# Kernel optimization log

Hardware: AMD Instinct MI355X
Metric: run time of the kernel (lower is better)

## Reference

```python
import jax, jax.numpy as jnp
import numpy as np

N_USER, N_ITEM, N_KNOW, HIDDEN, BATCH = 200000, 20000, 128, 256, 16384
N_EDGES = 2 * N_KNOW - 3  # chain edges (k-1,k) k=1..K-1 then skip edges (k-2,k) k=2..K-1


def setup_inputs() -> dict:
    key = jax.random.key(0)
    ks = jax.random.split(key, 12)
    return {
        'user_ids': jax.random.randint(ks[0], (BATCH,), 0, N_USER),
        'item_ids': jax.random.randint(ks[1], (BATCH,), 0, N_ITEM),
        'item_know': (jax.random.uniform(ks[2], (BATCH, N_KNOW)) < 0.5).astype(jnp.float32),
        'priori': jax.random.normal(ks[3], (N_USER, N_KNOW), jnp.float32),
        'condi_p': jax.random.normal(ks[4], (N_USER, N_EDGES), jnp.float32),
        'condi_n': jax.random.normal(ks[5], (N_USER, N_EDGES), jnp.float32),
        'item_diff_w': jax.random.normal(ks[6], (N_ITEM, N_KNOW), jnp.float32),
        'item_disc_w': jax.random.normal(ks[7], (N_ITEM, 1), jnp.float32),
        'Wu': jax.random.normal(ks[8], (HIDDEN, N_KNOW), jnp.float32) * 0.05,
        'bu': jax.random.normal(ks[9], (HIDDEN,), jnp.float32) * 0.05,
        'Wi': jax.random.normal(ks[10], (HIDDEN, N_KNOW), jnp.float32) * 0.05,
        'bi': jax.random.normal(ks[11], (HIDDEN,), jnp.float32) * 0.05,
    }


def _posterior(bp, bcp, bcn):
    # bp: [B,K] sigmoid(priori rows); bcp/bcn: [B,E] sigmoid(condi rows).
    # Topological DAG propagation. For node k the torch code sums over all
    # 2^len_p predecessor bitmasks of prod_j(mask_j*margin_p_j + (1-mask_j)*margin_n_j),
    # which factorizes exactly to prod_j(margin_p_j + margin_n_j) (same math).
    K = bp.shape[1]
    p0 = bp[:, 0]                               # node 0: no predecessors
    p1 = bcp[:, 0] * p0 + bcn[:, 0] * (1.0 - p0)  # node 1: pred {0}, exponent 1/1
    # nodes k>=2 have sorted preds {k-2, k-1}; edge (k-1,k) -> col k-1, edge (k-2,k) -> col (K-1)+(k-2)
    cp_b, cn_b = bcp[:, 1:K - 1].T, bcn[:, 1:K - 1].T      # (k-1,k) edges, [K-2,B]
    cp_a, cn_a = bcp[:, K - 1:].T, bcn[:, K - 1:].T        # (k-2,k) edges, [K-2,B]

    def step(carry, x):
        p_km2, p_km1 = carry
        cpa, cna, cpb, cnb = x
        # pow(condi, 1/len_p) with len_p=2 -> sqrt
        ta = jnp.sqrt(cpa) * p_km2 + jnp.sqrt(cna) * (1.0 - p_km2)
        tb = jnp.sqrt(cpb) * p_km1 + jnp.sqrt(cnb) * (1.0 - p_km1)
        pk = ta * tb
        return (p_km1, pk), pk

    _, rest = jax.lax.scan(step, (p0, p1), (cp_a, cn_a, cp_b, cn_b))  # rest: [K-2,B]
    return jnp.concatenate([p0[:, None], p1[:, None], rest.T], axis=1)  # [B,K]


def reference(user_ids, item_ids, item_know, priori, condi_p, condi_n,
              item_diff_w, item_disc_w, Wu, bu, Wi, bi):
    bp = jax.nn.sigmoid(priori[user_ids])      # [B,K]
    bcp = jax.nn.sigmoid(condi_p[user_ids])    # [B,E]
    bcn = jax.nn.sigmoid(condi_n[user_ids])
    mastery = _posterior(bp, bcp, bcn)         # [B,K]
    idiff = jax.nn.sigmoid(item_diff_w[item_ids])  # [B,K]
    idisc = jax.nn.sigmoid(item_disc_w[item_ids])  # [B,1]
    user_factor = jnp.tanh((mastery * item_know) @ Wu.T + bu)      # [B,H]
    item_factor = jax.nn.sigmoid((idiff * item_know) @ Wi.T + bi)  # [B,H]
    # mirt2pl: 1/(1+exp(-sum(u*i) + offset)) == sigmoid(sum - offset)
    logits = jnp.sum(user_factor * item_factor, axis=1, keepdims=True) - idisc
    return jax.nn.sigmoid(logits)  # [B,1]
```

## Files before the change

### kernel.cpp

```cpp
#include <hip/hip_runtime.h>

#define BATCH   16384
#define NKNOW   128
#define NEDGE   253
#define RPB     16

typedef __attribute__((ext_vector_type(8))) short  s16x8;
typedef __attribute__((ext_vector_type(4))) float  f32x4;
typedef __attribute__((ext_vector_type(4))) int    i32x4;

typedef unsigned short u16;
typedef unsigned int   u32;
typedef unsigned long long u64;

__device__ __forceinline__ float sigm(float x) { return 1.0f / (1.0f + __expf(-x)); }

__device__ __forceinline__ u16 f2bf_rn(float x) {
    u32 u = __float_as_uint(x);
    u += 0x7FFFu + ((u >> 16) & 1u);
    return (u16)(u >> 16);
}
__device__ __forceinline__ float bf2f(u16 h) { return __uint_as_float(((u32)h) << 16); }

__global__ __launch_bounds__(256, 4) void prep2(
    const int*   __restrict__ user_ids,
    const int*   __restrict__ item_ids,
    const float* __restrict__ item_know,
    const float* __restrict__ priori,
    const float* __restrict__ condi_p,
    const float* __restrict__ condi_n,
    const float* __restrict__ item_diff_w,
    const float* __restrict__ Wu,
    const float* __restrict__ Wi,
    u16*         __restrict__ wsp,
    u32*         __restrict__ mhi32,
    u32*         __restrict__ mlo32,
    u16*         __restrict__ dhi,
    u16*         __restrict__ dlo)
{
    __shared__ float4 sP[16][127];
    __shared__ uint4  sMask[16];

    const int tid = threadIdx.x;
    const int wid = tid >> 6, j = tid & 63;
    const int r0  = blockIdx.x * 16;

    #pragma unroll 2
    for (int q = 0; q < 4; ++q) {
        const int r = wid * 4 + q, row = r0 + r;
        const int uid = user_ids[row], iid = item_ids[row];
        const float* cp = condi_p + (size_t)uid * NEDGE;
        const float* cn = condi_n + (size_t)uid * NEDGE;
        const float* kw = item_know   + (size_t)row * NKNOW;
        const float* dw = item_diff_w + (size_t)iid * NKNOW;

        float a0p = cp[127 + j], a0n = cn[127 + j], b0p = cp[1 + j], b0n = cn[1 + j];
        float a1p = 0.f, a1n = 0.f, b1p = 0.f, b1n = 0.f;
        if (j < 62) { a1p = cp[191 + j]; a1n = cn[191 + j]; b1p = cp[65 + j]; b1n = cn[65 + j]; }
        float k0 = kw[j], k1 = kw[64 + j];
        float d0 = dw[j], d1 = dw[64 + j];

        float4 sA;
        sA.x = sqrtf(sigm(a0p)); sA.y = sqrtf(sigm(a0n));
        sA.z = sqrtf(sigm(b0p)); sA.w = sqrtf(sigm(b0n));
        sP[r][1 + j] = sA;
        if (j < 62) {
            float4 sB;
            sB.x = sqrtf(sigm(a1p)); sB.y = sqrtf(sigm(a1n));
            sB.z = sqrtf(sigm(b1p)); sB.w = sqrtf(sigm(b1n));
            sP[r][65 + j] = sB;
        }

        float dv0 = sigm(d0) * k0, dv1 = sigm(d1) * k1;
        u16 h0 = f2bf_rn(dv0), h1 = f2bf_rn(dv1);
        dhi[(size_t)row * NKNOW + j]      = h0;
        dhi[(size_t)row * NKNOW + 64 + j] = h1;
        dlo[(size_t)row * NKNOW + j]      = f2bf_rn(dv0 - bf2f(h0));
        dlo[(size_t)row * NKNOW + 64 + j] = f2bf_rn(dv1 - bf2f(h1));

        u64 m0 = __ballot(k0 > 0.5f);
        u64 m1 = __ballot(k1 > 0.5f);
        if (j == 0) {
            float4 hd;
            hd.x = sigm(cp[0]); hd.y = sigm(cn[0]);
            hd.z = sigm(priori[(size_t)uid * NKNOW]); hd.w = 0.f;
            sP[r][0] = hd;
            uint4 mm; mm.x = (u32)m0; mm.y = (u32)(m0 >> 32);
            mm.z = (u32)m1; mm.w = (u32)(m1 >> 32);
            sMask[r] = mm;
        }
    }

    if (blockIdx.x < 256) {
        int i = blockIdx.x * 256 + tid;
        bool isU = i < 32768;
        int  jj  = isU ? i : i - 32768;
        float w  = isU ? Wu[jj] : Wi[jj];
        u16 h = f2bf_rn(w);
        u16 l = f2bf_rn(w - bf2f(h));
        int base = isU ? 0 : 65536;
        wsp[base + jj]         = h;
        wsp[base + 32768 + jj] = l;
    }
    __syncthreads();

    if (tid < 16) {
        const int r = tid, row = r0 + r;
        uint4 mm = sMask[r];
        const u64 b0 = (u64)mm.x | ((u64)mm.y << 32);
        const u64 b1 = (u64)mm.z | ((u64)mm.w << 32);
        u32* mh = mhi32 + (size_t)row * 64;
        u32* ml = mlo32 + (size_t)row * 64;

        float4 h = sP[r][0];
        float p0 = h.z;
        float p1 = fmaf(p0, h.x - h.y, h.y);
        {
            float v0 = (b0 & 1ull) ? p0 : 0.f;
            float v1 = (b0 & 2ull) ? p1 : 0.f;
            u16 q0 = f2bf_rn(v0), q1 = f2bf_rn(v1);
            mh[0] = (u32)q0 | ((u32)q1 << 16);
            ml[0] = (u32)f2bf_rn(v0 - bf2f(q0)) | ((u32)f2bf_rn(v1 - bf2f(q1)) << 16);
        }

        float pm2 = p0, pm1 = p1, pendm = 0.f;
        float4 A[7], Bv[7];

#define LOADB(buf, bi_)                                               \
    _Pragma("unroll")                                                 \
    for (int t = 0; t < 7; ++t) buf[t] = sP[r][1 + 7 * (bi_) + t];

#define STEPS(buf, bi_)                                               \
    _Pragma("unroll")                                                 \
    for (int t = 0; t < 7; ++t) {                                     \
        const int k = 2 + 7 * (bi_) + t;                              \
        float4 s = buf[t];                                            \
        float ta = fmaf(pm2, s.x - s.y, s.y);                         \
        float tb = fmaf(pm1, s.z - s.w, s.w);                         \
        float pk = ta * tb;                                           \
        bool bit = (k < 64) ? ((b0 >> k) & 1ull) : ((b1 >> (k - 64)) & 1ull); \
        float pkm = bit ? pk : 0.f;                                   \
        if (k & 1) {                                                  \
            u16 q0 = f2bf_rn(pendm), q1 = f2bf_rn(pkm);               \
            mh[k >> 1] = (u32)q0 | ((u32)q1 << 16);                   \
            ml[k >> 1] = (u32)f2bf_rn(pendm - bf2f(q0)) |             \
                         ((u32)f2bf_rn(pkm - bf2f(q1)) << 16);        \
        } else pendm = pkm;                                           \
        pm2 = pm1; pm1 = pk;                                          \
    }
        LOADB(A, 0);
        LOADB(Bv, 1);  STEPS(A, 0);
        LOADB(A, 2);   STEPS(Bv, 1);
        LOADB(Bv, 3);  STEPS(A, 2);
        LOADB(A, 4);   STEPS(Bv, 3);
        LOADB(Bv, 5);  STEPS(A, 4);
        LOADB(A, 6);   STEPS(Bv, 5);
        LOADB(Bv, 7);  STEPS(A, 6);
        LOADB(A, 8);   STEPS(Bv, 7);
        LOADB(Bv, 9);  STEPS(A, 8);
        LOADB(A, 10);  STEPS(Bv, 9);
        LOADB(Bv, 11); STEPS(A, 10);
        LOADB(A, 12);  STEPS(Bv, 11);
        LOADB(Bv, 13); STEPS(A, 12);
        LOADB(A, 14);  STEPS(Bv, 13);
        LOADB(Bv, 15); STEPS(A, 14);
        LOADB(A, 16);  STEPS(Bv, 15);
        LOADB(Bv, 17); STEPS(A, 16);
        STEPS(Bv, 17);
#undef LOADB
#undef STEPS
    }
}

__global__ __launch_bounds__(256, 2) void gemm_ncd(
    const int*   __restrict__ item_ids,
    const float* __restrict__ item_disc_w,
    const float* __restrict__ bu,
    const float* __restrict__ bi,
    const u16*   __restrict__ wsp,
    const u32*   __restrict__ mhi32,
    const u32*   __restrict__ mlo32,
    const u32*   __restrict__ dhi32,
    const u32*   __restrict__ dlo32,
    float*       __restrict__ out)
{
    __shared__ float sRed[4][32];

    const int tid  = threadIdx.x;
    const int lane = tid & 63;
    const int wid  = tid >> 6;
    const int l15  = lane & 15, lq = lane >> 4;
    const int r0   = blockIdx.x * 32;

    const u16* WuH = wsp;
    const u16* WuL = wsp + 32768;
    const u16* WiH = wsp + 65536;
    const u16* WiL = wsp + 98304;

    float rowsum[2][4] = {{0.f,0.f,0.f,0.f},{0.f,0.f,0.f,0.f}};

    #pragma unroll 1
    for (int t = 0; t < 4; ++t) {
        const int hcol = wid * 64 + t * 16 + l15;
        s16x8 uh[4], ul[4], ih[4], il[4];
        #pragma unroll
        for (int kc = 0; kc < 4; ++kc) {
            const int ke = kc * 32 + lq * 8;
            uh[kc] = *(const s16x8*)(WuH + hcol * NKNOW + ke);
            ul[kc] = *(const s16x8*)(WuL + hcol * NKNOW + ke);
            ih[kc] = *(const s16x8*)(WiH + hcol * NKNOW + ke);
            il[kc] = *(const s16x8*)(WiL + hcol * NKNOW + ke);
        }
        const float bub = bu[hcol], bib = bi[hcol];

        #pragma unroll
        for (int rg = 0; rg < 2; ++rg) {
            const int row = r0 + rg * 16 + l15;
            f32x4 accU = {0.f, 0.f, 0.f, 0.f};
            f32x4 accV = {0.f, 0.f, 0.f, 0.f};
            #pragma unroll
            for (int kc = 0; kc < 4; ++kc) {
                const int aoff = row * 64 + kc * 16 + lq * 4;
                s16x8 mh = *(const s16x8*)(mhi32 + aoff);
                s16x8 mlv = *(const s16x8*)(mlo32 + aoff);
                s16x8 dh = *(const s16x8*)(dhi32 + aoff);
                s16x8 dl = *(const s16x8*)(dlo32 + aoff);
                accU = __builtin_amdgcn_mfma_f32_16x16x32_bf16(mh, uh[kc], accU, 0, 0, 0);
                accU = __builtin_amdgcn_mfma_f32_16x16x32_bf16(mh, ul[kc], accU, 0, 0, 0);
                accU = __builtin_amdgcn_mfma_f32_16x16x32_bf16(mlv, uh[kc], accU, 0, 0, 0);
                accV = __builtin_amdgcn_mfma_f32_16x16x32_bf16(dh, ih[kc], accV, 0, 0, 0);
                accV = __builtin_amdgcn_mfma_f32_16x16x32_bf16(dh, il[kc], accV, 0, 0, 0);
                accV = __builtin_amdgcn_mfma_f32_16x16x32_bf16(dl, ih[kc], accV, 0, 0, 0);
            }
            #pragma unroll
            for (int j = 0; j < 4; ++j) {
                float x = accU[j] + bub;
                float u = 1.0f - 2.0f / (1.0f + __expf(2.0f * x));
                float v = sigm(accV[j] + bib);
                rowsum[rg][j] += u * v;
            }
        }
    }

    #pragma unroll
    for (int rg = 0; rg < 2; ++rg)
        #pragma unroll
        for (int j = 0; j < 4; ++j) {
            float v = rowsum[rg][j];
            v += __shfl_xor(v, 1);
            v += __shfl_xor(v, 2);
            v += __shfl_xor(v, 4);
            v += __shfl_xor(v, 8);
            if (l15 == 0) sRed[wid][rg * 16 + lq * 4 + j] = v;
        }
    __syncthreads();

    if (tid < 32) {
        const int row = r0 + tid;
        float s = sRed[0][tid] + sRed[1][tid] + sRed[2][tid] + sRed[3][tid];
        float disc = sigm(item_disc_w[item_ids[row]]);
        out[row] = sigm(s - disc);
    }
}

__device__ __forceinline__ int swz(int row, int kbyte) {
    return row * 256 + (kbyte ^ ((row & 7) << 4));
}
__device__ __forceinline__ void store_pair(char* Mh, char* Ml, int r, int k0, float va, float vb) {
    int off = swz(r, k0 * 2);
    u16 ha = f2bf_rn(va); u16 la = f2bf_rn(va - bf2f(ha));
    u16 hb = f2bf_rn(vb); u16 lb = f2bf_rn(vb - bf2f(hb));
    *(u32*)(Mh + off) = (u32)ha | ((u32)hb << 16);
    *(u32*)(Ml + off) = (u32)la | ((u32)lb << 16);
}

__global__ void conv_w(const float* __restrict__ Wu, const float* __restrict__ Wi,
                       u16* __restrict__ wsp) {
    int i = blockIdx.x * 256 + threadIdx.x;
    bool isU = i < 32768;
    int  j   = isU ? i : i - 32768;
    float w  = isU ? Wu[j] : Wi[j];
    u16 h = f2bf_rn(w);
    u16 l = f2bf_rn(w - bf2f(h));
    int base = isU ? 0 : 65536;
    wsp[base + j]         = h;
    wsp[base + 32768 + j] = l;
}

__global__ __launch_bounds__(256, 3) void fused_ncd(
    const int*   __restrict__ user_ids,
    const int*   __restrict__ item_ids,
    const float* __restrict__ item_know,
    const float* __restrict__ priori,
    const float* __restrict__ condi_p,
    const float* __restrict__ condi_n,
    const float* __restrict__ item_diff_w,
    const float* __restrict__ item_disc_w,
    const float* __restrict__ bu,
    const float* __restrict__ bi,
    const u16* __restrict__ wsp,
    float*       __restrict__ out)
{
    __shared__ float sPair[RPB][508];
    __shared__ __align__(16) u16 sMhi[RPB * 128];
    __shared__ __align__(16) u16 sMlo[RPB * 128];
    __shared__ __align__(16) u16 sDhi[RPB * 128];
    __shared__ __align__(16) u16 sDlo[RPB * 128];
    __shared__ __align__(16) u16 sKmF[RPB * 128];
    __shared__ float sRed[4][RPB];
    __shared__ float sDisc[RPB];

    const int tid  = threadIdx.x;
    const int lane = tid & 63;
    const int wid  = tid >> 6;
    const int r0   = blockIdx.x * RPB;

    for (int rr = 0; rr < 4; ++rr) {
        const int r   = wid * 4 + rr;
        const int row = r0 + r;
        const int uid = user_ids[row];
        const int iid = item_ids[row];
        const float* cp = condi_p + (size_t)uid * NEDGE;
        const float* cn = condi_n + (size_t)uid * NEDGE;
        for (int e = lane; e < NEDGE; e += 64) {
            float p = sigm(cp[e]);
            float n = sigm(cn[e]);
            if (e >= 1) { p = sqrtf(p); n = sqrtf(n); }
            *(float2*)&sPair[r][2 * e] = make_float2(p, n);
        }
        const float* dw = item_diff_w + (size_t)iid * NKNOW;
        const float* kw = item_know   + (size_t)row * NKNOW;
        for (int e = lane; e < NKNOW; e += 64) {
            float kv = kw[e];
            float dv = sigm(dw[e]) * kv;
            u16 dh = f2bf_rn(dv);
            u16 dl = f2bf_rn(dv - bf2f(dh));
            int off = swz(r, 2 * e);
            *(u16*)((char*)sDhi + off) = dh;
            *(u16*)((char*)sDlo + off) = dl;
            *(u16*)((char*)sKmF + off) = (kv > 0.5f) ? (u16)0xFFFFu : (u16)0;
        }
    }
    __syncthreads();

    if (tid < RPB) {
        const int r   = tid;
        const int row = r0 + r;
        const int uid = user_ids[row];
        const int iid = item_ids[row];
        const float* P = &sPair[r][0];
        float p0 = sigm(priori[(size_t)uid * NKNOW]);
        float2 c0 = *(const float2*)&P[0];
        float p1 = c0.x * p0 + c0.y * (1.0f - p0);
        store_pair((char*)sMhi, (char*)sMlo, r, 0, p0, p1);
        float pm2 = p0, pm1 = p1, pev = 0.0f;
        for (int k = 2; k < NKNOW; ++k) {
            float2 a = *(const float2*)&P[2 * (125 + k)];
            float2 b = *(const float2*)&P[2 * (k - 1)];
            float ta = fmaf(pm2, a.x - a.y, a.y);
            float tb = fmaf(pm1, b.x - b.y, b.y);
            float pk = ta * tb;
            if (k & 1) store_pair((char*)sMhi, (char*)sMlo, r, k - 1, pev, pk);
            else       pev = pk;
            pm2 = pm1; pm1 = pk;
        }
        sDisc[r] = sigm(item_disc_w[iid]);
    }
    __syncthreads();

    const int l15 = lane & 15, lq = lane >> 4;
    const u16* WuH = wsp;
    const u16* WuL = wsp + 32768;
    const u16* WiH = wsp + 65536;
    const u16* WiL = wsp + 98304;

    float rowsum[4] = {0.f, 0.f, 0.f, 0.f};

    for (int t = 0; t < 4; ++t) {
        const int hcol = wid * 64 + t * 16 + l15;
        f32x4 accU = {0.f, 0.f, 0.f, 0.f};
        f32x4 accV = {0.f, 0.f, 0.f, 0.f};
        const u16* wuh = WuH + hcol * NKNOW;
        const u16* wul = WuL + hcol * NKNOW;
        const u16* wih = WiH + hcol * NKNOW;
        const u16* wil = WiL + hcol * NKNOW;
        #pragma unroll
        for (int kc = 0; kc < 4; ++kc) {
            const int offA = swz(l15, kc * 64 + lq * 16);
            const int ke   = kc * 32 + lq * 8;
            i32x4 km = *(const i32x4*)((const char*)sKmF + offA);
            i32x4 mh = *(const i32x4*)((const char*)sMhi + offA) & km;
            i32x4 ml = *(const i32x4*)((const char*)sMlo + offA) & km;
            s16x8 ah = *(s16x8*)&mh;
            s16x8 al = *(s16x8*)&ml;
            s16x8 bh = *(const s16x8*)((const char*)sDhi + offA);
            s16x8 bl = *(const s16x8*)((const char*)sDlo + offA);
            s16x8 uh = *(const s16x8*)(wuh + ke);
            s16x8 ul = *(const s16x8*)(wul + ke);
            s16x8 ih = *(const s16x8*)(wih + ke);
            s16x8 il = *(const s16x8*)(wil + ke);
            accU = __builtin_amdgcn_mfma_f32_16x16x32_bf16(ah, uh, accU, 0, 0, 0);
            accU = __builtin_amdgcn_mfma_f32_16x16x32_bf16(ah, ul, accU, 0, 0, 0);
            accU = __builtin_amdgcn_mfma_f32_16x16x32_bf16(al, uh, accU, 0, 0, 0);
            accV = __builtin_amdgcn_mfma_f32_16x16x32_bf16(bh, ih, accV, 0, 0, 0);
            accV = __builtin_amdgcn_mfma_f32_16x16x32_bf16(bh, il, accV, 0, 0, 0);
            accV = __builtin_amdgcn_mfma_f32_16x16x32_bf16(bl, ih, accV, 0, 0, 0);
        }
        const float bub = bu[hcol], bib = bi[hcol];
        #pragma unroll
        for (int j = 0; j < 4; ++j) {
            float x = accU[j] + bub;
            float u = 1.0f - 2.0f / (1.0f + __expf(2.0f * x));
            float v = sigm(accV[j] + bib);
            rowsum[j] += u * v;
        }
    }

    #pragma unroll
    for (int j = 0; j < 4; ++j) {
        float v = rowsum[j];
        v += __shfl_xor(v, 1);
        v += __shfl_xor(v, 2);
        v += __shfl_xor(v, 4);
        v += __shfl_xor(v, 8);
        if (l15 == 0) sRed[wid][lq * 4 + j] = v;
    }
    __syncthreads();

    if (tid < RPB) {
        float logit = sRed[0][tid] + sRed[1][tid] + sRed[2][tid] + sRed[3][tid] - sDisc[tid];
        out[r0 + tid] = sigm(logit);
    }
}

extern "C" void kernel_launch(void* const* d_in, const int* in_sizes, int n_in,
                              void* d_out, int out_size, void* d_ws, size_t ws_size,
                              hipStream_t stream) {
    const int*   user_ids    = (const int*)  d_in[0];
    const int*   item_ids    = (const int*)  d_in[1];
    const float* item_know   = (const float*)d_in[2];
    const float* priori      = (const float*)d_in[3];
    const float* condi_p     = (const float*)d_in[4];
    const float* condi_n     = (const float*)d_in[5];
    const float* item_diff_w = (const float*)d_in[6];
    const float* item_disc_w = (const float*)d_in[7];
    const float* Wu          = (const float*)d_in[8];
    const float* bu          = (const float*)d_in[9];
    const float* Wi          = (const float*)d_in[10];
    const float* bi          = (const float*)d_in[11];
    float* out = (float*)d_out;

    char* base = (char*)d_ws;
    u16* wsp   = (u16*)base;
    u32* mhi32 = (u32*)(base + 0x0040000);
    u32* mlo32 = (u32*)(base + 0x0440000);
    u16* dhi   = (u16*)(base + 0x0840000);
    u16* dlo   = (u16*)(base + 0x0C40000);
    const size_t need = 0x1040000;

    if (ws_size >= need) {
        prep2<<<BATCH / 16, 256, 0, stream>>>(
            user_ids, item_ids, item_know, priori, condi_p, condi_n,
            item_diff_w, Wu, Wi, wsp, mhi32, mlo32, dhi, dlo);
        gemm_ncd<<<BATCH / 32, 256, 0, stream>>>(
            item_ids, item_disc_w, bu, bi, wsp,
            mhi32, mlo32, (const u32*)dhi, (const u32*)dlo, out);
    } else {
        conv_w<<<256, 256, 0, stream>>>(Wu, Wi, wsp);
        fused_ncd<<<BATCH / RPB, 256, 0, stream>>>(
            user_ids, item_ids, item_know, priori, condi_p, condi_n,
            item_diff_w, item_disc_w, bu, bi, wsp, out);
    }
}
```

Measured before the change: 55.58 us.

## Process one row per wave in prep kernel and stage mastery outputs in LDS

The prep kernel now handles 4 rows per block, one per wave, instead of 16 rows per block with a single 16-thread tail doing all the serial scans. Each wave's lane 0 runs its own row's 126-step recurrence, so four scans run in parallel per block across many more blocks. The mastery hi/lo results are written to shared memory and then stored with coalesced per-lane writes, replacing scattered per-thread global stores. The grid is four times larger, and the serial scan still leaves 63 of 64 lanes idle in each wave.

```diff
diff --git a/kernel.cpp b/kernel.cpp
--- a/kernel.cpp
+++ b/kernel.cpp
@@ -22,7 +22,7 @@
 }
 __device__ __forceinline__ float bf2f(u16 h) { return __uint_as_float(((u32)h) << 16); }
 
-__global__ __launch_bounds__(256, 4) void prep2(
+__global__ __launch_bounds__(256, 4) void prep3(
     const int*   __restrict__ user_ids,
     const int*   __restrict__ item_ids,
     const float* __restrict__ item_know,
@@ -38,58 +38,46 @@
     u16*         __restrict__ dhi,
     u16*         __restrict__ dlo)
 {
-    __shared__ float4 sP[16][127];
-    __shared__ uint4  sMask[16];
+    __shared__ float4 sP[4][127];
+    __shared__ u32    sM[4][64];
+    __shared__ u32    sL[4][64];
 
     const int tid = threadIdx.x;
     const int wid = tid >> 6, j = tid & 63;
-    const int r0  = blockIdx.x * 16;
-
-    #pragma unroll 2
-    for (int q = 0; q < 4; ++q) {
-        const int r = wid * 4 + q, row = r0 + r;
-        const int uid = user_ids[row], iid = item_ids[row];
-        const float* cp = condi_p + (size_t)uid * NEDGE;
-        const float* cn = condi_n + (size_t)uid * NEDGE;
-        const float* kw = item_know   + (size_t)row * NKNOW;
-        const float* dw = item_diff_w + (size_t)iid * NKNOW;
-
-        float a0p = cp[127 + j], a0n = cn[127 + j], b0p = cp[1 + j], b0n = cn[1 + j];
-        float a1p = 0.f, a1n = 0.f, b1p = 0.f, b1n = 0.f;
-        if (j < 62) { a1p = cp[191 + j]; a1n = cn[191 + j]; b1p = cp[65 + j]; b1n = cn[65 + j]; }
-        float k0 = kw[j], k1 = kw[64 + j];
-        float d0 = dw[j], d1 = dw[64 + j];
-
-        float4 sA;
-        sA.x = sqrtf(sigm(a0p)); sA.y = sqrtf(sigm(a0n));
-        sA.z = sqrtf(sigm(b0p)); sA.w = sqrtf(sigm(b0n));
-        sP[r][1 + j] = sA;
-        if (j < 62) {
-            float4 sB;
-            sB.x = sqrtf(sigm(a1p)); sB.y = sqrtf(sigm(a1n));
-            sB.z = sqrtf(sigm(b1p)); sB.w = sqrtf(sigm(b1n));
-            sP[r][65 + j] = sB;
-        }
-
-        float dv0 = sigm(d0) * k0, dv1 = sigm(d1) * k1;
-        u16 h0 = f2bf_rn(dv0), h1 = f2bf_rn(dv1);
-        dhi[(size_t)row * NKNOW + j]      = h0;
-        dhi[(size_t)row * NKNOW + 64 + j] = h1;
-        dlo[(size_t)row * NKNOW + j]      = f2bf_rn(dv0 - bf2f(h0));
-        dlo[(size_t)row * NKNOW + 64 + j] = f2bf_rn(dv1 - bf2f(h1));
-
-        u64 m0 = __ballot(k0 > 0.5f);
-        u64 m1 = __ballot(k1 > 0.5f);
-        if (j == 0) {
-            float4 hd;
-            hd.x = sigm(cp[0]); hd.y = sigm(cn[0]);
-            hd.z = sigm(priori[(size_t)uid * NKNOW]); hd.w = 0.f;
-            sP[r][0] = hd;
-            uint4 mm; mm.x = (u32)m0; mm.y = (u32)(m0 >> 32);
-            mm.z = (u32)m1; mm.w = (u32)(m1 >> 32);
-            sMask[r] = mm;
-        }
-    }
+    const int row = blockIdx.x * 4 + wid;
+    const int uid = user_ids[row], iid = item_ids[row];
+    const float* cp = condi_p + (size_t)uid * NEDGE;
+    const float* cn = condi_n + (size_t)uid * NEDGE;
+    const float* kw = item_know   + (size_t)row * NKNOW;
+    const float* dw = item_diff_w + (size_t)iid * NKNOW;
+
+    float a0p = cp[127 + j], a0n = cn[127 + j], b0p = cp[1 + j], b0n = cn[1 + j];
+    float a1p = 0.f, a1n = 0.f, b1p = 0.f, b1n = 0.f;
+    if (j < 62) { a1p = cp[191 + j]; a1n = cn[191 + j]; b1p = cp[65 + j]; b1n = cn[65 + j]; }
+    float k0 = kw[j], k1 = kw[64 + j];
+    float d0 = dw[j], d1 = dw[64 + j];
+    float c0p = cp[0], c0n = cn[0], pri = priori[(size_t)uid * NKNOW];
+
+    float4 sA;
+    sA.x = sqrtf(sigm(a0p)); sA.y = sqrtf(sigm(a0n));
+    sA.z = sqrtf(sigm(b0p)); sA.w = sqrtf(sigm(b0n));
+    sP[wid][1 + j] = sA;
+    if (j < 62) {
+        float4 sB;
+        sB.x = sqrtf(sigm(a1p)); sB.y = sqrtf(sigm(a1n));
+        sB.z = sqrtf(sigm(b1p)); sB.w = sqrtf(sigm(b1n));
+        sP[wid][65 + j] = sB;
+    }
+
+    float dv0 = sigm(d0) * k0, dv1 = sigm(d1) * k1;
+    u16 h0 = f2bf_rn(dv0), h1 = f2bf_rn(dv1);
+    dhi[(size_t)row * NKNOW + j]      = h0;
+    dhi[(size_t)row * NKNOW + 64 + j] = h1;
+    dlo[(size_t)row * NKNOW + j]      = f2bf_rn(dv0 - bf2f(h0));
+    dlo[(size_t)row * NKNOW + 64 + j] = f2bf_rn(dv1 - bf2f(h1));
+
+    const u64 b0m = __ballot(k0 > 0.5f);
+    const u64 b1m = __ballot(k1 > 0.5f);
 
     if (blockIdx.x < 256) {
         int i = blockIdx.x * 256 + tid;
@@ -104,23 +92,16 @@
     }
     __syncthreads();
 
-    if (tid < 16) {
-        const int r = tid, row = r0 + r;
-        uint4 mm = sMask[r];
-        const u64 b0 = (u64)mm.x | ((u64)mm.y << 32);
-        const u64 b1 = (u64)mm.z | ((u64)mm.w << 32);
-        u32* mh = mhi32 + (size_t)row * 64;
-        u32* ml = mlo32 + (size_t)row * 64;
-
-        float4 h = sP[r][0];
-        float p0 = h.z;
-        float p1 = fmaf(p0, h.x - h.y, h.y);
+    if (j == 0) {
+        const int w = wid;
+        float p0 = sigm(pri);
+        float p1 = fmaf(p0, sigm(c0p) - sigm(c0n), sigm(c0n));
         {
-            float v0 = (b0 & 1ull) ? p0 : 0.f;
-            float v1 = (b0 & 2ull) ? p1 : 0.f;
+            float v0 = (b0m & 1ull) ? p0 : 0.f;
+            float v1 = (b0m & 2ull) ? p1 : 0.f;
             u16 q0 = f2bf_rn(v0), q1 = f2bf_rn(v1);
-            mh[0] = (u32)q0 | ((u32)q1 << 16);
-            ml[0] = (u32)f2bf_rn(v0 - bf2f(q0)) | ((u32)f2bf_rn(v1 - bf2f(q1)) << 16);
+            sM[w][0] = (u32)q0 | ((u32)q1 << 16);
+            sL[w][0] = (u32)f2bf_rn(v0 - bf2f(q0)) | ((u32)f2bf_rn(v1 - bf2f(q1)) << 16);
         }
 
         float pm2 = p0, pm1 = p1, pendm = 0.f;
@@ -128,7 +109,7 @@
 
 #define LOADB(buf, bi_)                                               \
     _Pragma("unroll")                                                 \
-    for (int t = 0; t < 7; ++t) buf[t] = sP[r][1 + 7 * (bi_) + t];
+    for (int t = 0; t < 7; ++t) buf[t] = sP[w][1 + 7 * (bi_) + t];
 
 #define STEPS(buf, bi_)                                               \
     _Pragma("unroll")                                                 \
@@ -138,13 +119,13 @@
         float ta = fmaf(pm2, s.x - s.y, s.y);                         \
         float tb = fmaf(pm1, s.z - s.w, s.w);                         \
         float pk = ta * tb;                                           \
-        bool bit = (k < 64) ? ((b0 >> k) & 1ull) : ((b1 >> (k - 64)) & 1ull); \
+        bool bit = (k < 64) ? ((b0m >> k) & 1ull) : ((b1m >> (k - 64)) & 1ull); \
         float pkm = bit ? pk : 0.f;                                   \
         if (k & 1) {                                                  \
             u16 q0 = f2bf_rn(pendm), q1 = f2bf_rn(pkm);               \
-            mh[k >> 1] = (u32)q0 | ((u32)q1 << 16);                   \
-            ml[k >> 1] = (u32)f2bf_rn(pendm - bf2f(q0)) |             \
-                         ((u32)f2bf_rn(pkm - bf2f(q1)) << 16);        \
+            sM[w][k >> 1] = (u32)q0 | ((u32)q1 << 16);                \
+            sL[w][k >> 1] = (u32)f2bf_rn(pendm - bf2f(q0)) |          \
+                            ((u32)f2bf_rn(pkm - bf2f(q1)) << 16);     \
         } else pendm = pkm;                                           \
         pm2 = pm1; pm1 = pk;                                          \
     }
@@ -170,6 +151,10 @@
 #undef LOADB
 #undef STEPS
     }
+    __syncthreads();
+
+    mhi32[(size_t)row * 64 + j] = sM[wid][j];
+    mlo32[(size_t)row * 64 + j] = sL[wid][j];
 }
 
 __global__ __launch_bounds__(256, 2) void gemm_ncd(
@@ -459,7 +444,7 @@
     const size_t need = 0x1040000;
 
     if (ws_size >= need) {
-        prep2<<<BATCH / 16, 256, 0, stream>>>(
+        prep3<<<BATCH / 4, 256, 0, stream>>>(
             user_ids, item_ids, item_know, priori, condi_p, condi_n,
             item_diff_w, Wu, Wi, wsp, mhi32, mlo32, dhi, dlo);
         gemm_ncd<<<BATCH / 32, 256, 0, stream>>>(
```

Result: slower. 93.37 us (+68.0%).
